# Kernel optimization log

Measured on AMD Instinct MI355X. Metric: run time of the kernel, lower is better.

## Reference

```python
import jax, jax.numpy as jnp
import numpy as np


def setup_inputs() -> dict:
    key = jax.random.key(0)
    k1, k2, k3 = jax.random.split(key, 3)
    B, Cin, Cout, L, K = 16, 64, 64, 65536, 3
    return {
        "x": jax.random.normal(k1, (B, Cin, L), dtype=jnp.float32),
        "alpha": jnp.zeros((1, Cin, 1), dtype=jnp.float32),
        "weight": jax.random.normal(k2, (Cout, Cin, K), dtype=jnp.float32),
        "weight_scale": jnp.ones((Cout, 1, 1), dtype=jnp.float32),
        "bias": jax.random.normal(k3, (Cout,), dtype=jnp.float32),
        "beta": jnp.ones((1, Cout, 1), dtype=jnp.float32),
        "gamma": jnp.zeros((1, Cout, 1), dtype=jnp.float32),
        "zeta": jnp.zeros((1, Cout, 1), dtype=jnp.float32),
    }


def _rsign(x, alpha):
    # forward: sign(x - alpha) in {-1,+1}; backward: identity w.r.t. x (STE)
    signed = jnp.where(x >= alpha, 1.0, -1.0).astype(x.dtype)
    return x + jax.lax.stop_gradient(signed - x)


def _clipped_ste_sign(w):
    # forward: sign(w); backward: grad passes only where |w| <= 1 (Bi-RealNet)
    w_bin = jnp.sign(w)
    mask = (jnp.abs(w) <= 1.0).astype(w.dtype)
    wm = w * mask
    return jax.lax.stop_gradient(w_bin) + wm - jax.lax.stop_gradient(wm)


def _rprelu(x, beta, gamma, zeta):
    xs = x - gamma
    return jnp.where(x > gamma, xs + zeta, beta * xs + zeta)


def reference(x, alpha, weight, weight_scale, bias, beta, gamma, zeta):
    # RSign -> scaled binary conv1d (stride=1, pad=1) -> RPReLU
    xb = _rsign(x, alpha)                        # [B,Cin,L], values +-1
    wb = _clipped_ste_sign(weight) * weight_scale  # [Cout,Cin,K]
    y = jax.lax.conv_general_dilated(
        xb, wb, window_strides=(1,), padding=[(1, 1)],
        dimension_numbers=("NCH", "OIH", "NCH"))  # [B,Cout,L]
    y = y + bias[None, :, None]
    return _rprelu(y, beta, gamma, zeta)
```

## Files before the change

### kernel.cpp

```cpp
#include <hip/hip_runtime.h>

#define LLEN 65536
#define CIN 64
#define COUT 64
#define LTILE 1024

typedef float f32x4 __attribute__((ext_vector_type(4)));
typedef unsigned long long u64;

struct __align__(64) WRec {
    u64 p0, p1, p2;
    float A;
    float S;
    float Bv, G, Z;
    float f0, f2;
    float pad[3];
};

__global__ void pack_weights(const float* __restrict__ w,
                             const float* __restrict__ wscale,
                             const float* __restrict__ bias,
                             const float* __restrict__ beta,
                             const float* __restrict__ gamma,
                             const float* __restrict__ zeta,
                             WRec* __restrict__ rec) {
    int co = threadIdx.x;
    if (co >= COUT) return;
    u64 p[3];
    int nnz[3], ntot = 0;
    for (int k = 0; k < 3; ++k) {
        u64 pos = 0ull, nz = 0ull;
        for (int ci = 0; ci < CIN; ++ci) {
            float wv = w[co * (CIN * 3) + ci * 3 + k];
            pos |= ((u64)(wv > 0.0f)) << ci;
            nz  |= ((u64)(wv != 0.0f)) << ci;
        }
        p[k] = pos;
        nnz[k] = __popcll(nz);
        ntot += nnz[k];
    }
    WRec r;
    float s = wscale[co];
    r.p0 = p[0]; r.p1 = p[1]; r.p2 = p[2];
    r.A  = s * (float)ntot + bias[co];
    r.S  = -2.0f * s;
    r.Bv = beta[co]; r.G = gamma[co]; r.Z = zeta[co];
    r.f0 = 0.5f * (float)nnz[0];
    r.f2 = 0.5f * (float)nnz[2];
    r.pad[0] = r.pad[1] = r.pad[2] = 0.0f;
    rec[co] = r;
}

__device__ __forceinline__ float rprelu(float y, float B, float G, float Z) {
    float xs = y - G;
    return (y > G) ? (xs + Z) : fmaf(B, xs, Z);
}

template <int EDGE>
__device__ __forceinline__ void co_loop(const WRec* __restrict__ rec,
                                        u64 xq0, u64 xq1, u64 xq2,
                                        u64 xq3, u64 xq4, u64 xq5,
                                        bool fixlane, float* __restrict__ outp) {
    #pragma unroll 4
    for (int co = 0; co < COUT; ++co) {
        const WRec r = rec[co];
        float fx = (float)(__popcll(xq0 ^ r.p0) + __popcll(xq1 ^ r.p1)
                         + __popcll(xq2 ^ r.p2));
        float fy = (float)(__popcll(xq1 ^ r.p0) + __popcll(xq2 ^ r.p1)
                         + __popcll(xq3 ^ r.p2));
        float fz = (float)(__popcll(xq2 ^ r.p0) + __popcll(xq3 ^ r.p1)
                         + __popcll(xq4 ^ r.p2));
        float fw = (float)(__popcll(xq3 ^ r.p0) + __popcll(xq4 ^ r.p1)
                         + __popcll(xq5 ^ r.p2));
        if (EDGE == 1 && fixlane)
            fx = (float)(__popcll(xq1 ^ r.p1) + __popcll(xq2 ^ r.p2)) + r.f0;
        if (EDGE == 2 && fixlane)
            fw = (float)(__popcll(xq3 ^ r.p0) + __popcll(xq4 ^ r.p1)) + r.f2;
        f32x4 o;
        o.x = rprelu(fmaf(r.S, fx, r.A), r.Bv, r.G, r.Z);
        o.y = rprelu(fmaf(r.S, fy, r.A), r.Bv, r.G, r.Z);
        o.z = rprelu(fmaf(r.S, fz, r.A), r.Bv, r.G, r.Z);
        o.w = rprelu(fmaf(r.S, fw, r.A), r.Bv, r.G, r.Z);
        __builtin_nontemporal_store(o, (f32x4*)(outp + (size_t)co * LLEN));
    }
}

__global__ void __launch_bounds__(256, 4) bconv_kernel(
        const float* __restrict__ x,
        const float* __restrict__ alpha,
        const WRec* __restrict__ rec,
        float* __restrict__ out) {
    const int lane = threadIdx.x & 63;
    const int wid  = threadIdx.x >> 6;
    const int b = blockIdx.y;
    const int wbase = blockIdx.x * LTILE + wid * 256;
    const int l = wbase + lane * 4;
    const float* xrow = x + (size_t)b * CIN * LLEN;

    const float alv = alpha[lane];
    const int llo = wbase - 1, lhi = wbase + 256;
    float vlo = 0.0f, vhi = 0.0f;
    if (llo >= 0)   vlo = xrow[(size_t)lane * LLEN + llo];
    if (lhi < LLEN) vhi = xrow[(size_t)lane * LLEN + lhi];

    const float* xb = xrow + l;
    u64 w0 = 0, w1 = 0, w2 = 0, w3 = 0;
    #pragma unroll 16
    for (int ci = 0; ci < CIN; ++ci) {
        const f32x4 v = *(const f32x4*)(xb + (size_t)ci * LLEN);
        const float a = alpha[ci];
        w0 |= ((u64)(v.x >= a)) << ci;
        w1 |= ((u64)(v.y >= a)) << ci;
        w2 |= ((u64)(v.z >= a)) << ci;
        w3 |= ((u64)(v.w >= a)) << ci;
    }

    const u64 halo_lo = __ballot(vlo >= alv);
    const u64 halo_hi = __ballot(vhi >= alv);

    u64 up = (u64)__shfl_up((long long)w3, 1);
    u64 dn = (u64)__shfl_down((long long)w0, 1);
    const u64 xq0 = (lane == 0)  ? halo_lo : up;
    const u64 xq1 = w0, xq2 = w1, xq3 = w2, xq4 = w3;
    const u64 xq5 = (lane == 63) ? halo_hi : dn;

    float* outp = out + (size_t)b * COUT * LLEN + l;

    if (blockIdx.x == 0)
        co_loop<1>(rec, xq0, xq1, xq2, xq3, xq4, xq5, threadIdx.x == 0, outp);
    else if (blockIdx.x == gridDim.x - 1)
        co_loop<2>(rec, xq0, xq1, xq2, xq3, xq4, xq5, threadIdx.x == 255, outp);
    else
        co_loop<0>(rec, xq0, xq1, xq2, xq3, xq4, xq5, false, outp);
}

extern "C" void kernel_launch(void* const* d_in, const int* in_sizes, int n_in,
                              void* d_out, int out_size, void* d_ws, size_t ws_size,
                              hipStream_t stream) {
    const float* x      = (const float*)d_in[0];
    const float* alpha  = (const float*)d_in[1];
    const float* w      = (const float*)d_in[2];
    const float* wscale = (const float*)d_in[3];
    const float* bias   = (const float*)d_in[4];
    const float* beta   = (const float*)d_in[5];
    const float* gamma  = (const float*)d_in[6];
    const float* zeta   = (const float*)d_in[7];
    float* out = (float*)d_out;

    WRec* rec = (WRec*)d_ws;

    pack_weights<<<1, 64, 0, stream>>>(w, wscale, bias, beta, gamma, zeta, rec);

    dim3 grid(LLEN / LTILE, 16);
    bconv_kernel<<<grid, 256, 0, stream>>>(x, alpha, rec, out);
}
```

Measured before the change: 110.8 us.

## Split binarization of x into separate packing kernel before bit-conv compute

The fused kernel is split in two. A new pack_x kernel thresholds x against alpha and writes 64-bit channel masks into a padded workspace row. bconv_compute then reads six neighbouring masks directly, replacing the per-wave halo loads, ballots and shuffles. The aim is to simplify the compute kernel and separate the read-heavy and write-heavy phases. The cost is an extra kernel launch, a round trip of the packed bits through global memory, and no overlap between reading x and writing the output.

```diff
diff --git a/kernel.cpp b/kernel.cpp
--- a/kernel.cpp
+++ b/kernel.cpp
@@ -7,6 +7,8 @@
 
 typedef float f32x4 __attribute__((ext_vector_type(4)));
 typedef unsigned long long u64;
+
+#define BROW (LLEN + 2)
 
 struct __align__(64) WRec {
     u64 p0, p1, p2;
@@ -51,6 +53,29 @@
     rec[co] = r;
 }
 
+__global__ void __launch_bounds__(256) pack_x(
+        const float* __restrict__ x,
+        const float* __restrict__ alpha,
+        u64* __restrict__ bits) {
+    const int t = threadIdx.x;
+    const int b = blockIdx.y;
+    const int l0 = blockIdx.x * LTILE + 4 * t;
+    const float* xb = x + (size_t)b * CIN * LLEN + l0;
+
+    u64 w0 = 0, w1 = 0, w2 = 0, w3 = 0;
+    #pragma unroll 16
+    for (int ci = 0; ci < CIN; ++ci) {
+        const f32x4 v = *(const f32x4*)(xb + (size_t)ci * LLEN);
+        const float a = alpha[ci];
+        w0 |= ((u64)(v.x >= a)) << ci;
+        w1 |= ((u64)(v.y >= a)) << ci;
+        w2 |= ((u64)(v.z >= a)) << ci;
+        w3 |= ((u64)(v.w >= a)) << ci;
+    }
+    u64* dst = bits + (size_t)b * BROW + l0 + 1;
+    dst[0] = w0; dst[1] = w1; dst[2] = w2; dst[3] = w3;
+}
+
 __device__ __forceinline__ float rprelu(float y, float B, float G, float Z) {
     float xs = y - G;
     return (y > G) ? (xs + Z) : fmaf(B, xs, Z);
@@ -85,51 +110,24 @@
     }
 }
 
-__global__ void __launch_bounds__(256, 4) bconv_kernel(
-        const float* __restrict__ x,
-        const float* __restrict__ alpha,
+__global__ void __launch_bounds__(256) bconv_compute(
+        const u64* __restrict__ bits,
         const WRec* __restrict__ rec,
         float* __restrict__ out) {
-    const int lane = threadIdx.x & 63;
-    const int wid  = threadIdx.x >> 6;
+    const int t = threadIdx.x;
     const int b = blockIdx.y;
-    const int wbase = blockIdx.x * LTILE + wid * 256;
-    const int l = wbase + lane * 4;
-    const float* xrow = x + (size_t)b * CIN * LLEN;
+    const int l0 = blockIdx.x * LTILE + 4 * t;
 
-    const float alv = alpha[lane];
-    const int llo = wbase - 1, lhi = wbase + 256;
-    float vlo = 0.0f, vhi = 0.0f;
-    if (llo >= 0)   vlo = xrow[(size_t)lane * LLEN + llo];
-    if (lhi < LLEN) vhi = xrow[(size_t)lane * LLEN + lhi];
+    const u64* src = bits + (size_t)b * BROW + l0;
+    const u64 xq0 = src[0], xq1 = src[1], xq2 = src[2],
+              xq3 = src[3], xq4 = src[4], xq5 = src[5];
 
-    const float* xb = xrow + l;
-    u64 w0 = 0, w1 = 0, w2 = 0, w3 = 0;
-    #pragma unroll 16
-    for (int ci = 0; ci < CIN; ++ci) {
-        const f32x4 v = *(const f32x4*)(xb + (size_t)ci * LLEN);
-        const float a = alpha[ci];
-        w0 |= ((u64)(v.x >= a)) << ci;
-        w1 |= ((u64)(v.y >= a)) << ci;
-        w2 |= ((u64)(v.z >= a)) << ci;
-        w3 |= ((u64)(v.w >= a)) << ci;
-    }
-
-    const u64 halo_lo = __ballot(vlo >= alv);
-    const u64 halo_hi = __ballot(vhi >= alv);
-
-    u64 up = (u64)__shfl_up((long long)w3, 1);
-    u64 dn = (u64)__shfl_down((long long)w0, 1);
-    const u64 xq0 = (lane == 0)  ? halo_lo : up;
-    const u64 xq1 = w0, xq2 = w1, xq3 = w2, xq4 = w3;
-    const u64 xq5 = (lane == 63) ? halo_hi : dn;
-
-    float* outp = out + (size_t)b * COUT * LLEN + l;
+    float* outp = out + (size_t)b * COUT * LLEN + l0;
 
     if (blockIdx.x == 0)
-        co_loop<1>(rec, xq0, xq1, xq2, xq3, xq4, xq5, threadIdx.x == 0, outp);
+        co_loop<1>(rec, xq0, xq1, xq2, xq3, xq4, xq5, t == 0, outp);
     else if (blockIdx.x == gridDim.x - 1)
-        co_loop<2>(rec, xq0, xq1, xq2, xq3, xq4, xq5, threadIdx.x == 255, outp);
+        co_loop<2>(rec, xq0, xq1, xq2, xq3, xq4, xq5, t == 255, outp);
     else
         co_loop<0>(rec, xq0, xq1, xq2, xq3, xq4, xq5, false, outp);
 }
@@ -148,9 +146,11 @@
     float* out = (float*)d_out;
 
     WRec* rec = (WRec*)d_ws;
+    u64* bits = (u64*)((char*)d_ws + 4096);
 
     pack_weights<<<1, 64, 0, stream>>>(w, wscale, bias, beta, gamma, zeta, rec);
 
     dim3 grid(LLEN / LTILE, 16);
-    bconv_kernel<<<grid, 256, 0, stream>>>(x, alpha, rec, out);
+    pack_x<<<grid, 256, 0, stream>>>(x, alpha, bits);
+    bconv_compute<<<grid, 256, 0, stream>>>(bits, rec, out);
 }
```

Result: slower. 121.6 us (+9.7%).
